# Performance work log

Hardware: AMD Instinct MI355X
Metric: run time of the kernel (lower is better)

The kernel has to match this reference:

```python
import jax, jax.numpy as jnp
import numpy as np

N = 100000      # nodes
E = 1600000     # edges (avg degree 16)
F = 64          # input node features
H = 128         # hidden channels
R = 20          # num relations (edge types)
G = 64          # graphs in batch
C = 10          # num classes
L = 2           # num RGCN layers
EPS = 1e-5      # BatchNorm eps


def setup_inputs() -> dict:
    key = jax.random.key(0)
    ks = jax.random.split(key, 14)
    s = 0.05
    return {
        "x": jax.random.normal(ks[0], (N, F), jnp.float32),
        "edge_index": jax.random.randint(ks[1], (2, E), 0, N, jnp.int32),
        "edge_type": jax.random.randint(ks[2], (E,), 0, R, jnp.int32),
        "batch": jnp.sort(jax.random.randint(ks[3], (N,), 0, G, jnp.int32)),
        # params
        "w_in": jax.random.normal(ks[4], (F, H), jnp.float32) * s,
        "b_in": jnp.zeros((H,), jnp.float32),
        "rel_w": jax.random.normal(ks[5], (L, R, H, H), jnp.float32) * s,
        "root_w": jax.random.normal(ks[6], (L, H, H), jnp.float32) * s,
        "conv_b": jnp.zeros((L, H), jnp.float32),
        "bn_g": jnp.ones((L, H), jnp.float32),
        "bn_b": jnp.zeros((L, H), jnp.float32),
        "w_out": jax.random.normal(ks[7], (H, C), jnp.float32) * s,
        "b_out": jnp.zeros((C,), jnp.float32),
    }


def reference(x, edge_index, edge_type, batch, w_in, b_in, rel_w, root_w,
              conv_b, bn_g, bn_b, w_out, b_out):
    # input MLP (dropout is identity in eval)
    h = jax.nn.relu(x @ w_in + b_in)

    src, dst = edge_index[0], edge_index[1]
    # per-(dst,relation) in-degree for RGCNConv mean aggregation
    comb = dst * R + edge_type                             # [E]
    cnt = jax.ops.segment_sum(jnp.ones((E,), jnp.float32), comb,
                              num_segments=N * R)
    edge_norm = (1.0 / jnp.maximum(cnt, 1.0))[comb]        # [E]

    for l in range(L):
        msg = h[src] * edge_norm[:, None]                  # [E, H] normalized source feats
        out = h @ root_w[l] + conv_b[l]                    # root/self transform + bias
        for r in range(R):
            mask = (edge_type == r).astype(h.dtype)        # [E]
            agg = jax.ops.segment_sum(msg * mask[:, None], dst,
                                      num_segments=N)      # [N, H] per-relation mean
            out = out + agg @ rel_w[l, r]
        # BatchNorm1d (training-mode batch statistics over nodes)
        mu = out.mean(axis=0)
        var = out.var(axis=0)
        out = (out - mu) * jax.lax.rsqrt(var + EPS) * bn_g[l] + bn_b[l]
        h = jax.nn.relu(out)                               # dropout = identity (eval)

    # global mean pool over graphs
    sums = jax.ops.segment_sum(h, batch, num_segments=G)   # [G, H]
    counts = jax.ops.segment_sum(jnp.ones((N,), h.dtype), batch, num_segments=G)
    pooled = sums / jnp.maximum(counts, 1.0)[:, None]

    logits = pooled @ w_out + b_out                        # [G, C]
    return jax.nn.sigmoid(logits)
```

## Files before the change

kernel.cpp:

```cpp
#include <hip/hip_runtime.h>

#define N_NODES 100000
#define E_EDGES 1600000
#define F_IN    64
#define H_DIM   128
#define R_REL   20
#define G_GRAPHS 64
#define C_CLASSES 10
#define L_LAYERS 2
#define BN_EPS  1e-5f
#define RN      (R_REL * N_NODES)

typedef unsigned short u16;
typedef unsigned int   u32;
typedef __attribute__((ext_vector_type(8))) short short8;
typedef __attribute__((ext_vector_type(4))) float f32x4;

static __device__ __forceinline__ float bf2f(u16 u) {
    u32 b = ((u32)u) << 16;
    return __builtin_bit_cast(float, b);
}
static __device__ __forceinline__ u16 f2bf(float f) {
    u32 x = __builtin_bit_cast(u32, f);
    u32 r = x + 0x7fff + ((x >> 16) & 1);
    return (u16)(r >> 16);
}


__global__ void count_kernel(const int* __restrict__ ei, const int* __restrict__ et,
                             int* __restrict__ hist) {
    for (int e = blockIdx.x * blockDim.x + threadIdx.x; e < E_EDGES;
         e += gridDim.x * blockDim.x) {
        int t = et[e];
        int d = ei[E_EDGES + e];
        atomicAdd(&hist[t * N_NODES + d], 1);
    }
}

__global__ void scan1_kernel(const int* __restrict__ in, int* __restrict__ out,
                             int* __restrict__ part, int n) {
    __shared__ int s[256];
    int t = threadIdx.x;
    int base = blockIdx.x * 1024;
    int v[4]; int sum = 0;
#pragma unroll
    for (int j = 0; j < 4; ++j) {
        int i = base + t * 4 + j;
        v[j] = (i < n) ? in[i] : 0;
        sum += v[j];
    }
    s[t] = sum;
    __syncthreads();
    for (int off = 1; off < 256; off <<= 1) {
        int x = (t >= off) ? s[t - off] : 0;
        __syncthreads();
        s[t] += x;
        __syncthreads();
    }
    if (t == 255) part[blockIdx.x] = s[255];
    int run = s[t] - sum;
#pragma unroll
    for (int j = 0; j < 4; ++j) {
        int i = base + t * 4 + j;
        if (i < n) out[i] = run;
        run += v[j];
    }
}

__global__ void scan2_kernel(int* __restrict__ part, int nb) {
    __shared__ int s[256];
    int t = threadIdx.x;
    int loc[8]; int sum = 0;
#pragma unroll
    for (int j = 0; j < 8; ++j) {
        int i = t * 8 + j;
        loc[j] = (i < nb) ? part[i] : 0;
        sum += loc[j];
    }
    s[t] = sum;
    __syncthreads();
    for (int off = 1; off < 256; off <<= 1) {
        int x = (t >= off) ? s[t - off] : 0;
        __syncthreads();
        s[t] += x;
        __syncthreads();
    }
    int run = s[t] - sum;
#pragma unroll
    for (int j = 0; j < 8; ++j) {
        int i = t * 8 + j;
        if (i < nb) part[i] = run;
        run += loc[j];
    }
}

__global__ void scan3_kernel(int* __restrict__ out, int* __restrict__ cur2,
                             const int* __restrict__ part, int n) {
    for (int i = blockIdx.x * blockDim.x + threadIdx.x; i < n;
         i += gridDim.x * blockDim.x) {
        int v = out[i] + part[i >> 10];
        out[i] = v;
        cur2[i] = v;
    }
}

__global__ void finalize_kernel(int* __restrict__ off2) {
    if (threadIdx.x == 0) off2[RN] = E_EDGES;
}

__global__ void bucket_kernel(const int* __restrict__ ei, const int* __restrict__ et,
                              int* __restrict__ cur2, int2* __restrict__ epair) {
    for (int e = blockIdx.x * blockDim.x + threadIdx.x; e < E_EDGES;
         e += gridDim.x * blockDim.x) {
        int t = et[e];
        int s = ei[e];
        int d = ei[E_EDGES + e];
        int pos = atomicAdd(&cur2[t * N_NODES + d], 1);
        epair[pos] = make_int2(s, d);
    }
}

template<int K>
__global__ void pack_w(const float* __restrict__ W, u16* __restrict__ Wp) {
    const float* w = W + (size_t)blockIdx.x * K * H_DIM;
    u16* p = Wp + (size_t)blockIdx.x * K * H_DIM;
    for (int o = threadIdx.x; o < K * H_DIM; o += blockDim.x) {
        int j  = o & 7;
        int l  = (o >> 3) & 63;
        int ct = (o >> 9) & 7;
        int kt = o >> 12;
        int k  = kt * 32 + (l >> 4) * 8 + j;
        int n  = ct * 16 + (l & 15);
        p[o] = f2bf(w[(size_t)k * H_DIM + n]);
    }
}

__global__ void cvt_bf16_kernel(const float* __restrict__ in, u16* __restrict__ out, int n4) {
    for (int i = blockIdx.x * blockDim.x + threadIdx.x; i < n4;
         i += gridDim.x * blockDim.x) {
        float4 v = ((const float4*)in)[i];
        ushort4 o;
        o.x = f2bf(v.x); o.y = f2bf(v.y); o.z = f2bf(v.z); o.w = f2bf(v.w);
        ((ushort4*)out)[i] = o;
    }
}

template<int K, bool RELU, bool HASBIAS, bool OUTBF16>
__global__ __launch_bounds__(256)
void mfma_dense(const u16* __restrict__ A, const u16* __restrict__ Wp,
                const float* __restrict__ bias, void* __restrict__ OutV, int M) {
    constexpr int CH = K / 8;
    __shared__ u16 Ws[K * H_DIM];
    __shared__ u16 As[64 * H_DIM];

    for (int o = threadIdx.x; o < K * H_DIM / 8; o += 256)
        ((short8*)Ws)[o] = ((const short8*)Wp)[o];

    const int lane = threadIdx.x & 63;
    const int wave = threadIdx.x >> 6;
    const int l15  = lane & 15;
    const int kgrp = lane >> 4;
    const int arow = wave * 16 + l15;

    for (int tb = blockIdx.x * 64; tb < M; tb += gridDim.x * 64) {
        __syncthreads();
        for (int o = threadIdx.x; o < 64 * CH; o += 256) {
            int row = o / CH, cc = o % CH;
            int grow = tb + row;
            short8 v = {0,0,0,0,0,0,0,0};
            if (grow < M) v = *(const short8*)&A[(size_t)grow * K + cc * 8];
            *(short8*)&As[row * K + ((cc ^ (row & 7)) * 8)] = v;
        }
        __syncthreads();

        f32x4 acc[8];
#pragma unroll
        for (int i = 0; i < 8; ++i) {
            acc[i][0] = 0.f; acc[i][1] = 0.f; acc[i][2] = 0.f; acc[i][3] = 0.f;
        }
#pragma unroll
        for (int kt = 0; kt < K / 32; ++kt) {
            short8 af = *(const short8*)&As[arow * K + (((kt * 4 + kgrp) ^ (arow & 7)) * 8)];
#pragma unroll
            for (int ct = 0; ct < 8; ++ct) {
                short8 bf = *(const short8*)&Ws[(((kt * 8 + ct) * 64) + lane) * 8];
                acc[ct] = __builtin_amdgcn_mfma_f32_16x16x32_bf16(af, bf, acc[ct], 0, 0, 0);
            }
        }

        if (OUTBF16) {
            __syncthreads();
#pragma unroll
            for (int ct = 0; ct < 8; ++ct) {
#pragma unroll
                for (int r = 0; r < 4; ++r) {
                    int row = wave * 16 + kgrp * 4 + r;
                    int col = ct * 16 + l15;
                    float v = acc[ct][r];
                    if (HASBIAS) v += bias[col];
                    if (RELU)    v = fmaxf(v, 0.f);
                    As[row * H_DIM + ((((col >> 3) ^ (row & 7)) << 3) | (col & 7))] = f2bf(v);
                }
            }
            __syncthreads();
            u16* Out = (u16*)OutV;
            for (int o = threadIdx.x; o < 64 * 16; o += 256) {
                int row = o >> 4, cc = o & 15;
                int grow = tb + row;
                if (grow < M)
                    *(short8*)&Out[(size_t)grow * H_DIM + cc * 8] =
                        *(const short8*)&As[row * H_DIM + ((cc ^ (row & 7)) << 3)];
            }
        } else {
            float* Out = (float*)OutV;
#pragma unroll
            for (int ct = 0; ct < 8; ++ct) {
#pragma unroll
                for (int r = 0; r < 4; ++r) {
                    int grow = tb + wave * 16 + kgrp * 4 + r;
                    if (grow < M) {
                        float v = acc[ct][r];
                        if (HASBIAS) v += bias[ct * 16 + l15];
                        if (RELU)    v = fmaxf(v, 0.f);
                        Out[(size_t)grow * H_DIM + ct * 16 + l15] = v;
                    }
                }
            }
        }
    }
}

__global__ __launch_bounds__(512, 4)
void rgcn_conv(const u16* __restrict__ h, const u16* __restrict__ Wrel,
               const u16* __restrict__ Wroot, const float* __restrict__ bias,
               const int2* __restrict__ epair, const int* __restrict__ off2,
               float* __restrict__ outb, float* __restrict__ bn_sums) {
    __shared__ int offs[R_REL][129];
    __shared__ u16 Ws[H_DIM * H_DIM];
    __shared__ u16 Abf[128 * H_DIM];
    __shared__ float bnS[H_DIM], bnSS[H_DIM];

    const int d0 = blockIdx.x * 128;
    for (int i = threadIdx.x; i < R_REL * 129; i += 512) {
        int r = i / 129, j = i % 129;
        offs[r][j] = off2[r * N_NODES + min(d0 + j, N_NODES)];
    }
    if (threadIdx.x < H_DIM) { bnS[threadIdx.x] = 0.f; bnSS[threadIdx.x] = 0.f; }

    const int lane = threadIdx.x & 63;
    const int wv   = threadIdx.x >> 6;
    const int l15  = lane & 15;
    const int kgrp = lane >> 4;
    const int arow = wv * 16 + l15;
    const u32* h2  = (const u32*)h;
    u32* Ab32 = (u32*)Abf;

    f32x4 acc[8];
#pragma unroll
    for (int i = 0; i < 8; ++i) {
        acc[i][0] = 0.f; acc[i][1] = 0.f; acc[i][2] = 0.f; acc[i][3] = 0.f;
    }

    int estart = 0, eend = 0;
    int dd[16];
    u32 rv[16];

    auto flushrow = [&](int dcur, int cnt, float f0, float f1) {
        float nm = 1.0f / (float)cnt;
        int dr = dcur - d0;
        u32 pk = (u32)f2bf(f0 * nm) | ((u32)f2bf(f1 * nm) << 16);
        Ab32[dr * 64 + ((((lane >> 2) ^ (dr & 7)) << 2) | (lane & 3))] = pk;
    };

    auto prefetch = [&](int rr) {
        if (rr < R_REL) {
            estart = __builtin_amdgcn_readfirstlane(offs[rr][wv * 16]);
            eend   = __builtin_amdgcn_readfirstlane(offs[rr][wv * 16 + 16]);
            if (eend > estart) {
                const int last = eend - 1;
                int ss[16];
#pragma unroll
                for (int j = 0; j < 16; ++j) {
                    int2 pr = epair[min(estart + j, last)];
                    ss[j] = pr.x; dd[j] = pr.y;
                }
#pragma unroll
                for (int j = 0; j < 16; ++j)
                    rv[j] = h2[(size_t)ss[j] * 64 + lane];
            }
        }
    };

    __syncthreads();
    prefetch(0);

    for (int r = 0; r < R_REL; ++r) {
        const bool active = (offs[r][0] != offs[r][128]);
        if (active) {
            for (int o = threadIdx.x; o < H_DIM * H_DIM / 8; o += 512)
                ((short8*)Ws)[o] = ((const short8*)(Wrel + (size_t)r * H_DIM * H_DIM))[o];
#pragma unroll
            for (int i = 0; i < 16; ++i)
                Ab32[(wv * 16 + i) * 64 + lane] = 0u;
            if (eend > estart) {
                int dcur = -1, cnt = 0;
                float f0 = 0.f, f1 = 0.f;
#pragma unroll
                for (int j = 0; j < 16; ++j) {
                    if (estart + j < eend) {
                        if (dd[j] != dcur) {
                            if (dcur >= 0) flushrow(dcur, cnt, f0, f1);
                            dcur = dd[j]; f0 = 0.f; f1 = 0.f; cnt = 0;
                        }
                        f0 += bf2f((u16)(rv[j] & 0xffff));
                        f1 += bf2f((u16)(rv[j] >> 16));
                        cnt++;
                    }
                }
                for (int e = estart + 16; e < eend; e += 16) {
                    const int last = eend - 1;
                    int ss2[16], dd2[16];
                    u32 rv2[16];
#pragma unroll
                    for (int j = 0; j < 16; ++j) {
                        int2 pr = epair[min(e + j, last)];
                        ss2[j] = pr.x; dd2[j] = pr.y;
                    }
#pragma unroll
                    for (int j = 0; j < 16; ++j)
                        rv2[j] = h2[(size_t)ss2[j] * 64 + lane];
#pragma unroll
                    for (int j = 0; j < 16; ++j) {
                        if (e + j < eend) {
                            if (dd2[j] != dcur) {
                                if (dcur >= 0) flushrow(dcur, cnt, f0, f1);
                                dcur = dd2[j]; f0 = 0.f; f1 = 0.f; cnt = 0;
                            }
                            f0 += bf2f((u16)(rv2[j] & 0xffff));
                            f1 += bf2f((u16)(rv2[j] >> 16));
                            cnt++;
                        }
                    }
                }
                if (dcur >= 0) flushrow(dcur, cnt, f0, f1);
            }
        }
        __syncthreads();
        prefetch(r + 1);
        if (active) {
#pragma unroll
            for (int kt = 0; kt < 4; ++kt) {
                short8 af = *(const short8*)&Abf[arow * H_DIM + (((kt * 4 + kgrp) ^ (arow & 7)) * 8)];
#pragma unroll
                for (int ct = 0; ct < 8; ++ct) {
                    short8 bf = *(const short8*)&Ws[(((kt * 8 + ct) * 64) + lane) * 8];
                    acc[ct] = __builtin_amdgcn_mfma_f32_16x16x32_bf16(af, bf, acc[ct], 0, 0, 0);
                }
            }
        }
        __syncthreads();
    }

    for (int o = threadIdx.x; o < H_DIM * H_DIM / 8; o += 512)
        ((short8*)Ws)[o] = ((const short8*)Wroot)[o];
    __syncthreads();
    {
        const int hrow = min(d0 + arow, N_NODES - 1);
#pragma unroll
        for (int kt = 0; kt < 4; ++kt) {
            short8 af = *(const short8*)&h[(size_t)hrow * H_DIM + kt * 32 + kgrp * 8];
#pragma unroll
            for (int ct = 0; ct < 8; ++ct) {
                short8 bf = *(const short8*)&Ws[(((kt * 8 + ct) * 64) + lane) * 8];
                acc[ct] = __builtin_amdgcn_mfma_f32_16x16x32_bf16(af, bf, acc[ct], 0, 0, 0);
            }
        }
    }

#pragma unroll
    for (int ct = 0; ct < 8; ++ct) {
        float bv = bias[ct * 16 + l15];
        float sl = 0.f, sq = 0.f;
#pragma unroll
        for (int rr = 0; rr < 4; ++rr) {
            int grow = d0 + wv * 16 + kgrp * 4 + rr;
            if (grow < N_NODES) {
                float v = acc[ct][rr] + bv;
                outb[(size_t)grow * H_DIM + ct * 16 + l15] = v;
                sl += v;
                sq += v * v;
            }
        }
        sl += __shfl_xor(sl, 16); sl += __shfl_xor(sl, 32);
        sq += __shfl_xor(sq, 16); sq += __shfl_xor(sq, 32);
        if (kgrp == 0) {
            atomicAdd(&bnS[ct * 16 + l15], sl);
            atomicAdd(&bnSS[ct * 16 + l15], sq);
        }
    }
    __syncthreads();
    if (threadIdx.x < H_DIM) {
        atomicAdd(&bn_sums[threadIdx.x], bnS[threadIdx.x]);
        atomicAdd(&bn_sums[H_DIM + threadIdx.x], bnSS[threadIdx.x]);
    }
}

__global__ void bn_apply(const float* __restrict__ X, const float* __restrict__ sums,
                         const float* __restrict__ gg, const float* __restrict__ bb,
                         u16* __restrict__ Hout) {
    __shared__ float sc[H_DIM], sh[H_DIM];
    if (threadIdx.x < H_DIM) {
        float mean = sums[threadIdx.x] * (1.0f / N_NODES);
        float var  = sums[H_DIM + threadIdx.x] * (1.0f / N_NODES) - mean * mean;
        float inv  = rsqrtf(var + BN_EPS) * gg[threadIdx.x];
        sc[threadIdx.x] = inv;
        sh[threadIdx.x] = bb[threadIdx.x] - mean * inv;
    }
    __syncthreads();
    int total = N_NODES * (H_DIM / 4);
    for (int idx = blockIdx.x * 256 + threadIdx.x; idx < total; idx += gridDim.x * 256) {
        float4 v = ((const float4*)X)[idx];
        int c = (idx & 31) << 2;
        ushort4 o;
        o.x = f2bf(fmaxf(v.x * sc[c + 0] + sh[c + 0], 0.f));
        o.y = f2bf(fmaxf(v.y * sc[c + 1] + sh[c + 1], 0.f));
        o.z = f2bf(fmaxf(v.z * sc[c + 2] + sh[c + 2], 0.f));
        o.w = f2bf(fmaxf(v.w * sc[c + 3] + sh[c + 3], 0.f));
        ((ushort4*)Hout)[idx] = o;
    }
}

__global__ void pool_kernel(const u16* __restrict__ Hf, const int* __restrict__ batch,
                            float* __restrict__ pool, float* __restrict__ pcnt) {
    int col  = threadIdx.x & 127;
    int half = threadIdx.x >> 7;
    int chunk = (N_NODES + gridDim.x - 1) / gridDim.x;
    int start = blockIdx.x * chunk;
    int end   = min(N_NODES, start + chunk);
    int curg = -1;
    float acc = 0.f, c = 0.f;
    for (int row = start + half; row < end; row += 2) {
        int g = batch[row];
        if (g != curg) {
            if (curg >= 0) {
                atomicAdd(&pool[curg * H_DIM + col], acc);
                if (col == 0) atomicAdd(&pcnt[curg], c);
            }
            curg = g; acc = 0.f; c = 0.f;
        }
        acc += bf2f(Hf[(size_t)row * H_DIM + col]);
        c += 1.f;
    }
    if (curg >= 0) {
        atomicAdd(&pool[curg * H_DIM + col], acc);
        if (col == 0) atomicAdd(&pcnt[curg], c);
    }
}

__global__ void logits_kernel(const float* __restrict__ pool, const float* __restrict__ pcnt,
                              const float* __restrict__ w_out, const float* __restrict__ b_out,
                              float* __restrict__ out) {
    int g = blockIdx.x;
    __shared__ float p[H_DIM];
    float cnt = fmaxf(pcnt[g], 1.0f);
    p[threadIdx.x] = pool[g * H_DIM + threadIdx.x] / cnt;
    __syncthreads();
    if (threadIdx.x < C_CLASSES) {
        float acc = b_out[threadIdx.x];
        for (int k = 0; k < H_DIM; ++k)
            acc += p[k] * w_out[k * C_CLASSES + threadIdx.x];
        out[g * C_CLASSES + threadIdx.x] = 1.0f / (1.0f + expf(-acc));
    }
}

static inline size_t align256(size_t x) { return (x + 255) & ~(size_t)255; }

extern "C" void kernel_launch(void* const* d_in, const int* in_sizes, int n_in,
                              void* d_out, int out_size, void* d_ws, size_t ws_size,
                              hipStream_t stream) {
    const float* x      = (const float*)d_in[0];
    const int*   ei     = (const int*)d_in[1];
    const int*   et     = (const int*)d_in[2];
    const int*   batch  = (const int*)d_in[3];
    const float* w_in   = (const float*)d_in[4];
    const float* b_in   = (const float*)d_in[5];
    const float* rel_w  = (const float*)d_in[6];
    const float* root_w = (const float*)d_in[7];
    const float* conv_b = (const float*)d_in[8];
    const float* bn_g   = (const float*)d_in[9];
    const float* bn_b   = (const float*)d_in[10];
    const float* w_out  = (const float*)d_in[11];
    const float* b_out  = (const float*)d_in[12];
    float* out = (float*)d_out;

    char* ws = (char*)d_ws;
    size_t off = 0;
    u16*   h_bf  = (u16*)(ws + off);  off += align256((size_t)N_NODES * H_DIM * 2);
    float* outb  = (float*)(ws + off); off += align256((size_t)N_NODES * H_DIM * 4);
    u16*   x_bf  = (u16*)(ws + off);  off += align256((size_t)N_NODES * F_IN * 2);
    int*   off2  = (int*)(ws + off);  off += align256((size_t)(RN + 1) * 4 + 256);
    int*   cur2  = (int*)(ws + off);  off += align256((size_t)RN * 4);
    int2*  e_pair = (int2*)(ws + off); off += align256((size_t)E_EDGES * 8 + 256);
    u16*   wp_in   = (u16*)(ws + off); off += align256((size_t)F_IN * H_DIM * 2);
    u16*   wp_root = (u16*)(ws + off); off += align256((size_t)L_LAYERS * H_DIM * H_DIM * 2);
    u16*   wp_rel  = (u16*)(ws + off); off += align256((size_t)L_LAYERS * R_REL * H_DIM * H_DIM * 2);
    int*   scan_part  = (int*)(ws + off); off += align256(2048 * 4);
    float* bn_sums    = (float*)(ws + off); off += align256(2 * H_DIM * 4);
    float* pool       = (float*)(ws + off); off += align256((size_t)G_GRAPHS * H_DIM * 4);
    float* pcnt       = (float*)(ws + off); off += 256;

    hipMemsetAsync(cur2, 0, (size_t)RN * 4, stream);
    count_kernel<<<1024, 256, 0, stream>>>(ei, et, cur2);
    const int NB = (RN + 1023) / 1024;
    scan1_kernel<<<NB, 256, 0, stream>>>(cur2, off2, scan_part, RN);
    scan2_kernel<<<1, 256, 0, stream>>>(scan_part, NB);
    scan3_kernel<<<2048, 256, 0, stream>>>(off2, cur2, scan_part, RN);
    finalize_kernel<<<1, 64, 0, stream>>>(off2);
    bucket_kernel<<<2048, 256, 0, stream>>>(ei, et, cur2, e_pair);

    cvt_bf16_kernel<<<2048, 256, 0, stream>>>(x, x_bf, N_NODES * F_IN / 4);
    pack_w<F_IN><<<1, 256, 0, stream>>>(w_in, wp_in);
    pack_w<H_DIM><<<L_LAYERS, 256, 0, stream>>>(root_w, wp_root);
    pack_w<H_DIM><<<L_LAYERS * R_REL, 256, 0, stream>>>(rel_w, wp_rel);

    mfma_dense<F_IN, true, true, true><<<dim3(640), 256, 0, stream>>>(
        x_bf, wp_in, b_in, h_bf, N_NODES);

    const int CONV_BLOCKS = (N_NODES + 127) / 128;
    for (int l = 0; l < L_LAYERS; ++l) {
        hipMemsetAsync(bn_sums, 0, 2 * H_DIM * 4, stream);
        rgcn_conv<<<dim3(CONV_BLOCKS), 512, 0, stream>>>(
            h_bf, wp_rel + (size_t)l * R_REL * H_DIM * H_DIM,
            wp_root + (size_t)l * H_DIM * H_DIM, conv_b + (size_t)l * H_DIM,
            e_pair, off2, outb, bn_sums);
        bn_apply<<<2048, 256, 0, stream>>>(outb, bn_sums,
                                           bn_g + (size_t)l * H_DIM,
                                           bn_b + (size_t)l * H_DIM, h_bf);
    }

    hipMemsetAsync(pool, 0, (size_t)G_GRAPHS * H_DIM * 4, stream);
    hipMemsetAsync(pcnt, 0, 256, stream);
    pool_kernel<<<512, 256, 0, stream>>>(h_bf, batch, pool, pcnt);
    logits_kernel<<<G_GRAPHS, 128, 0, stream>>>(pool, pcnt, w_out, b_out, out);
}
```

Measured before the change: 867.8 us.

## Make RGCN conv waves independent: read relation weights from global, drop barriers

The conv kernel now uses 64-node blocks of 256 threads and no longer stages the 32KB relation and root weight matrices in LDS. Each wave reads the packed weight fragments straight from global memory (L2-resident) and skips relations that have no edges for its own 16 rows, so the per-relation __syncthreads are removed. The software prefetch of the next relation's edge gather is also dropped. This aims to cut LDS usage, barrier stalls and redundant weight copies, at the cost of repeated global/L2 weight reads per wave and less latency hiding for the gathers.

```diff
diff --git a/kernel.cpp b/kernel.cpp
--- a/kernel.cpp
+++ b/kernel.cpp
@@ -230,19 +230,18 @@
     }
 }
 
-__global__ __launch_bounds__(512, 4)
+__global__ __launch_bounds__(256, 4)
 void rgcn_conv(const u16* __restrict__ h, const u16* __restrict__ Wrel,
                const u16* __restrict__ Wroot, const float* __restrict__ bias,
                const int2* __restrict__ epair, const int* __restrict__ off2,
                float* __restrict__ outb, float* __restrict__ bn_sums) {
-    __shared__ int offs[R_REL][129];
-    __shared__ u16 Ws[H_DIM * H_DIM];
-    __shared__ u16 Abf[128 * H_DIM];
+    __shared__ int offs[R_REL][65];
+    __shared__ u16 Abf[64 * H_DIM];
     __shared__ float bnS[H_DIM], bnSS[H_DIM];
 
-    const int d0 = blockIdx.x * 128;
-    for (int i = threadIdx.x; i < R_REL * 129; i += 512) {
-        int r = i / 129, j = i % 129;
+    const int d0 = blockIdx.x * 64;
+    for (int i = threadIdx.x; i < R_REL * 65; i += 256) {
+        int r = i / 65, j = i % 65;
         offs[r][j] = off2[r * N_NODES + min(d0 + j, N_NODES)];
     }
     if (threadIdx.x < H_DIM) { bnS[threadIdx.x] = 0.f; bnSS[threadIdx.x] = 0.f; }
@@ -261,10 +260,6 @@
         acc[i][0] = 0.f; acc[i][1] = 0.f; acc[i][2] = 0.f; acc[i][3] = 0.f;
     }
 
-    int estart = 0, eend = 0;
-    int dd[16];
-    u32 rv[16];
-
     auto flushrow = [&](int dcur, int cnt, float f0, float f1) {
         float nm = 1.0f / (float)cnt;
         int dr = dcur - d0;
@@ -272,98 +267,83 @@
         Ab32[dr * 64 + ((((lane >> 2) ^ (dr & 7)) << 2) | (lane & 3))] = pk;
     };
 
-    auto prefetch = [&](int rr) {
-        if (rr < R_REL) {
-            estart = __builtin_amdgcn_readfirstlane(offs[rr][wv * 16]);
-            eend   = __builtin_amdgcn_readfirstlane(offs[rr][wv * 16 + 16]);
-            if (eend > estart) {
-                const int last = eend - 1;
-                int ss[16];
+    __syncthreads();
+
+    for (int r = 0; r < R_REL; ++r) {
+        const int estart = __builtin_amdgcn_readfirstlane(offs[r][wv * 16]);
+        const int eend   = __builtin_amdgcn_readfirstlane(offs[r][wv * 16 + 16]);
+        if (eend <= estart) continue;
+
+#pragma unroll
+        for (int i = 0; i < 16; ++i)
+            Ab32[(wv * 16 + i) * 64 + lane] = 0u;
+
+        {
+            const int last = eend - 1;
+            int ss[16], dd[16];
+            u32 rv[16];
+#pragma unroll
+            for (int j = 0; j < 16; ++j) {
+                int2 pr = epair[min(estart + j, last)];
+                ss[j] = pr.x; dd[j] = pr.y;
+            }
+#pragma unroll
+            for (int j = 0; j < 16; ++j)
+                rv[j] = h2[(size_t)ss[j] * 64 + lane];
+
+            int dcur = -1, cnt = 0;
+            float f0 = 0.f, f1 = 0.f;
+#pragma unroll
+            for (int j = 0; j < 16; ++j) {
+                if (estart + j < eend) {
+                    if (dd[j] != dcur) {
+                        if (dcur >= 0) flushrow(dcur, cnt, f0, f1);
+                        dcur = dd[j]; f0 = 0.f; f1 = 0.f; cnt = 0;
+                    }
+                    f0 += bf2f((u16)(rv[j] & 0xffff));
+                    f1 += bf2f((u16)(rv[j] >> 16));
+                    cnt++;
+                }
+            }
+            for (int e = estart + 16; e < eend; e += 16) {
+                int ss2[16], dd2[16];
+                u32 rv2[16];
 #pragma unroll
                 for (int j = 0; j < 16; ++j) {
-                    int2 pr = epair[min(estart + j, last)];
-                    ss[j] = pr.x; dd[j] = pr.y;
+                    int2 pr = epair[min(e + j, last)];
+                    ss2[j] = pr.x; dd2[j] = pr.y;
                 }
 #pragma unroll
                 for (int j = 0; j < 16; ++j)
-                    rv[j] = h2[(size_t)ss[j] * 64 + lane];
-            }
-        }
-    };
-
-    __syncthreads();
-    prefetch(0);
-
-    for (int r = 0; r < R_REL; ++r) {
-        const bool active = (offs[r][0] != offs[r][128]);
-        if (active) {
-            for (int o = threadIdx.x; o < H_DIM * H_DIM / 8; o += 512)
-                ((short8*)Ws)[o] = ((const short8*)(Wrel + (size_t)r * H_DIM * H_DIM))[o];
-#pragma unroll
-            for (int i = 0; i < 16; ++i)
-                Ab32[(wv * 16 + i) * 64 + lane] = 0u;
-            if (eend > estart) {
-                int dcur = -1, cnt = 0;
-                float f0 = 0.f, f1 = 0.f;
+                    rv2[j] = h2[(size_t)ss2[j] * 64 + lane];
 #pragma unroll
                 for (int j = 0; j < 16; ++j) {
-                    if (estart + j < eend) {
-                        if (dd[j] != dcur) {
+                    if (e + j < eend) {
+                        if (dd2[j] != dcur) {
                             if (dcur >= 0) flushrow(dcur, cnt, f0, f1);
-                            dcur = dd[j]; f0 = 0.f; f1 = 0.f; cnt = 0;
+                            dcur = dd2[j]; f0 = 0.f; f1 = 0.f; cnt = 0;
                         }
-                        f0 += bf2f((u16)(rv[j] & 0xffff));
-                        f1 += bf2f((u16)(rv[j] >> 16));
+                        f0 += bf2f((u16)(rv2[j] & 0xffff));
+                        f1 += bf2f((u16)(rv2[j] >> 16));
                         cnt++;
                     }
                 }
-                for (int e = estart + 16; e < eend; e += 16) {
-                    const int last = eend - 1;
-                    int ss2[16], dd2[16];
-                    u32 rv2[16];
-#pragma unroll
-                    for (int j = 0; j < 16; ++j) {
-                        int2 pr = epair[min(e + j, last)];
-                        ss2[j] = pr.x; dd2[j] = pr.y;
-                    }
-#pragma unroll
-                    for (int j = 0; j < 16; ++j)
-                        rv2[j] = h2[(size_t)ss2[j] * 64 + lane];
-#pragma unroll
-                    for (int j = 0; j < 16; ++j) {
-                        if (e + j < eend) {
-                            if (dd2[j] != dcur) {
-                                if (dcur >= 0) flushrow(dcur, cnt, f0, f1);
-                                dcur = dd2[j]; f0 = 0.f; f1 = 0.f; cnt = 0;
-                            }
-                            f0 += bf2f((u16)(rv2[j] & 0xffff));
-                            f1 += bf2f((u16)(rv2[j] >> 16));
-                            cnt++;
-                        }
-                    }
-                }
-                if (dcur >= 0) flushrow(dcur, cnt, f0, f1);
-            }
-        }
-        __syncthreads();
-        prefetch(r + 1);
-        if (active) {
-#pragma unroll
-            for (int kt = 0; kt < 4; ++kt) {
-                short8 af = *(const short8*)&Abf[arow * H_DIM + (((kt * 4 + kgrp) ^ (arow & 7)) * 8)];
-#pragma unroll
-                for (int ct = 0; ct < 8; ++ct) {
-                    short8 bf = *(const short8*)&Ws[(((kt * 8 + ct) * 64) + lane) * 8];
-                    acc[ct] = __builtin_amdgcn_mfma_f32_16x16x32_bf16(af, bf, acc[ct], 0, 0, 0);
-                }
-            }
-        }
-        __syncthreads();
-    }
-
-    for (int o = threadIdx.x; o < H_DIM * H_DIM / 8; o += 512)
-        ((short8*)Ws)[o] = ((const short8*)Wroot)[o];
-    __syncthreads();
+            }
+            if (dcur >= 0) flushrow(dcur, cnt, f0, f1);
+        }
+
+        const u16* Wr = Wrel + (size_t)r * H_DIM * H_DIM;
+#pragma unroll
+        for (int kt = 0; kt < 4; ++kt) {
+            short8 af = *(const short8*)&Abf[arow * H_DIM + (((kt * 4 + kgrp) ^ (arow & 7)) * 8)];
+#pragma unroll
+            for (int ct = 0; ct < 8; ++ct) {
+                short8 bf = *(const short8*)&Wr[(((kt * 8 + ct) * 64) + lane) * 8];
+                acc[ct] = __builtin_amdgcn_mfma_f32_16x16x32_bf16(af, bf, acc[ct], 0, 0, 0);
+            }
+        }
+    }
+
     {
         const int hrow = min(d0 + arow, N_NODES - 1);
 #pragma unroll
@@ -371,7 +351,7 @@
             short8 af = *(const short8*)&h[(size_t)hrow * H_DIM + kt * 32 + kgrp * 8];
 #pragma unroll
             for (int ct = 0; ct < 8; ++ct) {
-                short8 bf = *(const short8*)&Ws[(((kt * 8 + ct) * 64) + lane) * 8];
+                short8 bf = *(const short8*)&Wroot[(((kt * 8 + ct) * 64) + lane) * 8];
                 acc[ct] = __builtin_amdgcn_mfma_f32_16x16x32_bf16(af, bf, acc[ct], 0, 0, 0);
             }
         }
@@ -526,10 +506,10 @@
     mfma_dense<F_IN, true, true, true><<<dim3(640), 256, 0, stream>>>(
         x_bf, wp_in, b_in, h_bf, N_NODES);
 
-    const int CONV_BLOCKS = (N_NODES + 127) / 128;
+    const int CONV_BLOCKS = (N_NODES + 63) / 64;
     for (int l = 0; l < L_LAYERS; ++l) {
         hipMemsetAsync(bn_sums, 0, 2 * H_DIM * 4, stream);
-        rgcn_conv<<<dim3(CONV_BLOCKS), 512, 0, stream>>>(
+        rgcn_conv<<<dim3(CONV_BLOCKS), 256, 0, stream>>>(
             h_bf, wp_rel + (size_t)l * R_REL * H_DIM * H_DIM,
             wp_root + (size_t)l * H_DIM * H_DIM, conv_b + (size_t)l * H_DIM,
             e_pair, off2, outb, bn_sums);
```

Measured after the change: 817.6 us. 5.8% less time.
